# Performance work log

Measured on AMD Instinct MI355X. Metric: run time of the kernel, lower is better.

## Reference

```python
import jax, jax.numpy as jnp
import numpy as np

EMB = 256  # embedding_dim


def setup_inputs() -> dict:
    key = jax.random.key(0)
    ks = jax.random.split(key, 9)
    B, S, D = 4, 4096, EMB
    inputs = jax.random.normal(ks[0], (B, S, 3 * D), dtype=jnp.float32)
    def dense(kw, kb, d_in, d_out):
        w = jax.random.normal(kw, (d_in, d_out), dtype=jnp.float32) / np.sqrt(d_in)
        b = jnp.zeros((d_out,), dtype=jnp.float32)
        return w, b
    wq, bq = dense(ks[1], ks[2], D, D)
    wk, bk = dense(ks[3], ks[4], D, D)
    wv, bv = dense(ks[5], ks[6], D, D)
    wo, bo = dense(ks[7], ks[8], D, D)
    return {"inputs": inputs, "wq": wq, "bq": bq, "wk": wk, "bk": bk,
            "wv": wv, "bv": bv, "wo": wo, "bo": bo}


def reference(inputs, wq, bq, wk, bk, wv, bv, wo, bo):
    # split last axis into q,k,v parts: [B,S,D] each
    q_in, k_in, v_in = jnp.split(inputs, 3, axis=-1)
    q = q_in @ wq + bq
    k = k_in @ wk + bk
    v = v_in @ wv + bv
    dk = jnp.asarray(k.shape[-1], dtype=jnp.float32)
    # unfused SDPA exactly as source: matmul -> scale -> softmax -> matmul
    logits = jnp.einsum('bsd,btd->bst', q, k) / jnp.sqrt(dk)  # [B,S,S]
    attn = jax.nn.softmax(logits, axis=-1)
    x = jnp.einsum('bst,btd->bsd', attn, v)
    return x @ wo + bo
```

## Files before the change

### kernel.cpp

```cpp
#include <hip/hip_runtime.h>

typedef _Float16 f16;
typedef _Float16 f16x4 __attribute__((ext_vector_type(4)));
typedef _Float16 f16x8 __attribute__((ext_vector_type(8)));
typedef float f32x4  __attribute__((ext_vector_type(4)));

#define MFMAH(a, b, c) __builtin_amdgcn_mfma_f32_16x16x32_f16(a, b, c, 0, 0, 0)

constexpr int D = 256;
constexpr int S = 4096;
constexpr int BATCH = 4;
constexpr int NROWS = BATCH * S;
constexpr float SCALE = 0.0625f;
constexpr size_t NE = (size_t)NROWS * D;

__device__ __forceinline__ void gll16(const void* g, void* l) {
  __builtin_amdgcn_global_load_lds(
      (const __attribute__((address_space(1))) unsigned int*)g,
      (__attribute__((address_space(3))) unsigned int*)l, 16, 0, 0);
}

__global__ __launch_bounds__(256)
void prep_wt_kernel(const float* __restrict__ wq, const float* __restrict__ wk,
                    const float* __restrict__ wv, const float* __restrict__ wo,
                    f16* __restrict__ Wt)
{
  const int m = blockIdx.y;
  const float* w = (m == 0) ? wq : (m == 1) ? wk : (m == 2) ? wv : wo;
  int id = blockIdx.x * 256 + threadIdx.x;
  int n = id >> 8, k = id & 255;
  Wt[((size_t)m << 16) + n * 256 + k] = (f16)w[k * 256 + n];
}

__global__ __launch_bounds__(256)
void qkv_mfma_kernel(const float* __restrict__ in, const f16* __restrict__ Wt,
                     const float* __restrict__ bq, const float* __restrict__ bk,
                     const float* __restrict__ bv,
                     f16* __restrict__ Qh, f16* __restrict__ Kf, f16* __restrict__ Vf)
{
  __shared__ __align__(16) char smem[32768];
  const int m = blockIdx.y;
  const int tid = threadIdx.x, lane = tid & 63, w = tid >> 6;
  const int l15 = lane & 15, quad = lane >> 4;
  const int row0 = blockIdx.x * 64 + w * 16;
  const f16* Wm = Wt + ((size_t)m << 16);
  const float* bias = (m == 0) ? bq : (m == 1) ? bk : bv;

  f16x8 af[8];
  {
    const float* arow = in + (size_t)(row0 + l15) * 768 + m * 256 + quad * 8;
#pragma unroll
    for (int kc = 0; kc < 8; ++kc) {
      float4 a0 = *(const float4*)(arow + kc * 32);
      float4 a1 = *(const float4*)(arow + kc * 32 + 4);
      f16x8 a;
      a[0] = (f16)a0.x; a[1] = (f16)a0.y; a[2] = (f16)a0.z; a[3] = (f16)a0.w;
      a[4] = (f16)a1.x; a[5] = (f16)a1.y; a[6] = (f16)a1.z; a[7] = (f16)a1.w;
      af[kc] = a;
    }
  }

  auto stageB = [&](int buf, int kc) {
    char* base = smem + buf * 16384;
#pragma unroll
    for (int i = 0; i < 4; ++i) {
      int ct = 4 * w + i;
      gll16(Wm + (ct * 16 + l15) * 256 + kc * 32 + quad * 8,
            base + ct * 1024 + lane * 16);
    }
  };

  f32x4 acc[16];
#pragma unroll
  for (int ct = 0; ct < 16; ++ct) acc[ct] = (f32x4){0.f, 0.f, 0.f, 0.f};

  stageB(0, 0);
  for (int kc = 0; kc < 8; ++kc) {
    __syncthreads();
    if (kc < 7) stageB((kc + 1) & 1, kc + 1);
    const char* Bb = smem + (kc & 1) * 16384;
#pragma unroll
    for (int ct = 0; ct < 16; ++ct) {
      f16x8 b = *(const f16x8*)(Bb + ct * 1024 + lane * 16);
      acc[ct] = MFMAH(af[kc], b, acc[ct]);
    }
  }
  __syncthreads();

  const int b_ = row0 >> 12;

  if (m == 0) {
    f16* ws = (f16*)(smem + w * 8192);
#pragma unroll
    for (int ct = 0; ct < 16; ++ct) {
      float bct = bias[ct * 16 + l15];
#pragma unroll
      for (int r = 0; r < 4; ++r)
        ws[(quad * 4 + r) * 256 + ct * 16 + l15] = (f16)((acc[ct][r] + bct) * SCALE);
    }
    f16* dst = Qh + (size_t)row0 * 256;
#pragma unroll
    for (int i = 0; i < 8; ++i)
      *(uint4*)(dst + lane * 8 + i * 512) = *(const uint4*)(ws + lane * 8 + i * 512);
  } else if (m == 1) {
    f16* ws = (f16*)(smem + w * 8192);
#pragma unroll
    for (int ct = 0; ct < 16; ++ct) {
      float bct = bias[ct * 16 + l15];
      int base = (ct >> 1) * 512 + ((ct & 1) * 2 + (l15 >> 3)) * 128 + (l15 & 7);
#pragma unroll
      for (int r = 0; r < 4; ++r)
        ws[base + (quad * 4 + r) * 8] = (f16)(acc[ct][r] + bct);
    }
    const int g = (row0 & 4095) >> 4;
    f16* dst = Kf + ((size_t)(b_ * 256 + g)) * 8 * 512;
#pragma unroll
    for (int i = 0; i < 8; ++i)
      *(uint4*)(dst + lane * 8 + i * 512) = *(const uint4*)(ws + lane * 8 + i * 512);
  } else {
    const int t = w & 1;
    f16* ws = (f16*)(smem + (w >> 1) * 16384);
#pragma unroll
    for (int ct = 0; ct < 16; ++ct) {
      float bct = bias[ct * 16 + l15];
      int base = ct * 512 + quad * 128 + l15 * 8 + t * 4;
#pragma unroll
      for (int r = 0; r < 4; ++r)
        ws[base + r] = (f16)(acc[ct][r] + bct);
    }
    __syncthreads();
    const int gv0 = ((blockIdx.x * 64) & 4095) >> 5;
    f16* dst = Vf + ((size_t)(b_ * 128 + gv0)) * 16 * 512;
    const f16* src = (const f16*)smem;
#pragma unroll
    for (int i = 0; i < 8; ++i)
      *(uint4*)(dst + tid * 8 + i * 2048) = *(const uint4*)(src + tid * 8 + i * 2048);
  }
}

__global__ __launch_bounds__(256, 2)
void attn6_kernel(const f16* __restrict__ Qh, const char* __restrict__ Kf,
                  const char* __restrict__ Vf,
                  f16* __restrict__ Pp, float* __restrict__ Mp, float* __restrict__ Lp)
{
  __shared__ __align__(16) char KVs[2][32768];

  const int tid = threadIdx.x, lane = tid & 63, w = tid >> 6;
  const int l15 = lane & 15, quad = lane >> 4;

  const int bx    = blockIdx.x;
  const int combo = bx & 15;
  const int b     = combo & 3;
  const int kz    = combo >> 2;
  const int qb    = bx >> 4;
  const int qrow0 = qb * 128 + w * 32;
  const int grow  = b * 4096 + qrow0;

  f16x8 qf[2][8];
#pragma unroll
  for (int sub = 0; sub < 2; ++sub) {
    const size_t qoff = (size_t)(grow + sub * 16 + l15) * 256 + quad * 8;
#pragma unroll
    for (int kc = 0; kc < 8; ++kc)
      qf[sub][kc] = *(const f16x8*)(Qh + qoff + kc * 32);
  }

  const char* kg[4];
  const char* vg[4];
#pragma unroll
  for (int i = 0; i < 4; ++i) {
    int f = 4 * w + i;
    kg[i] = Kf + (((size_t)(b * 256 + kz * 64 + (f >> 3))) * 8 + (f & 7)) * 1024
               + lane * 16;
    vg[i] = Vf + (((size_t)(b * 128 + kz * 32)) * 16 + f) * 1024 + lane * 16;
  }
  auto stage = [&](int buf) {
    char* base = &KVs[buf][0];
#pragma unroll
    for (int i = 0; i < 4; ++i) { gll16(kg[i], base + (4 * w + i) * 1024); kg[i] += 16384; }
#pragma unroll
    for (int i = 0; i < 4; ++i) { gll16(vg[i], base + 16384 + (4 * w + i) * 1024); vg[i] += 16384; }
  };

  f32x4 o0[16], o1[16];
#pragma unroll
  for (int ct = 0; ct < 16; ++ct) {
    o0[ct] = (f32x4){0.f, 0.f, 0.f, 0.f};
    o1[ct] = (f32x4){0.f, 0.f, 0.f, 0.f};
  }
  float m0 = -3.0e38f, m1 = -3.0e38f, l0 = 0.f, l1 = 0.f;

  stage(0);

  for (int it = 0; it < 32; ++it) {
    __syncthreads();
    if (it < 31) stage((it + 1) & 1);
    const char* Bf = &KVs[it & 1][0];

    f32x4 sA0 = (f32x4){0.f,0.f,0.f,0.f}, sB0 = (f32x4){0.f,0.f,0.f,0.f};
    f32x4 sA1 = (f32x4){0.f,0.f,0.f,0.f}, sB1 = (f32x4){0.f,0.f,0.f,0.f};
#pragma unroll
    for (int kc = 0; kc < 8; ++kc) {
      f16x8 kA = *(const f16x8*)(Bf + kc * 1024 + lane * 16);
      f16x8 kB = *(const f16x8*)(Bf + 8192 + kc * 1024 + lane * 16);
      sA0 = MFMAH(kA, qf[0][kc], sA0);
      sA1 = MFMAH(kA, qf[1][kc], sA1);
      sB0 = MFMAH(kB, qf[0][kc], sB0);
      sB1 = MFMAH(kB, qf[1][kc], sB1);
    }

    float mn0, mn1, al0, al1;
    f16x8 ph0, ph1;
    {
      float t = fmaxf(fmaxf(fmaxf(sA0[0], sA0[1]), fmaxf(sA0[2], sA0[3])),
                      fmaxf(fmaxf(sB0[0], sB0[1]), fmaxf(sB0[2], sB0[3])));
      t = fmaxf(t, __shfl_xor(t, 16));
      t = fmaxf(t, __shfl_xor(t, 32));
      mn0 = fmaxf(m0, t);
      al0 = __expf(m0 - mn0);
      float ps = 0.f;
#pragma unroll
      for (int r = 0; r < 4; ++r) {
        float pa = __expf(sA0[r] - mn0);
        float pb = __expf(sB0[r] - mn0);
        ph0[r] = (f16)pa;  ph0[r + 4] = (f16)pb;
        ps += pa + pb;
      }
      ps += __shfl_xor(ps, 16);
      ps += __shfl_xor(ps, 32);
      l0 = l0 * al0 + ps;
    }
    {
      float t = fmaxf(fmaxf(fmaxf(sA1[0], sA1[1]), fmaxf(sA1[2], sA1[3])),
                      fmaxf(fmaxf(sB1[0], sB1[1]), fmaxf(sB1[2], sB1[3])));
      t = fmaxf(t, __shfl_xor(t, 16));
      t = fmaxf(t, __shfl_xor(t, 32));
      mn1 = fmaxf(m1, t);
      al1 = __expf(m1 - mn1);
      float ps = 0.f;
#pragma unroll
      for (int r = 0; r < 4; ++r) {
        float pa = __expf(sA1[r] - mn1);
        float pb = __expf(sB1[r] - mn1);
        ph1[r] = (f16)pa;  ph1[r + 4] = (f16)pb;
        ps += pa + pb;
      }
      ps += __shfl_xor(ps, 16);
      ps += __shfl_xor(ps, 32);
      l1 = l1 * al1 + ps;
    }

    if (__any(mn0 > m0)) {
      float a0 = __shfl(al0, (quad << 2) + 0);
      float a1 = __shfl(al0, (quad << 2) + 1);
      float a2 = __shfl(al0, (quad << 2) + 2);
      float a3 = __shfl(al0, (quad << 2) + 3);
#pragma unroll
      for (int ct = 0; ct < 16; ++ct) {
        o0[ct][0] *= a0; o0[ct][1] *= a1; o0[ct][2] *= a2; o0[ct][3] *= a3;
      }
    }
    if (__any(mn1 > m1)) {
      float a0 = __shfl(al1, (quad << 2) + 0);
      float a1 = __shfl(al1, (quad << 2) + 1);
      float a2 = __shfl(al1, (quad << 2) + 2);
      float a3 = __shfl(al1, (quad << 2) + 3);
#pragma unroll
      for (int ct = 0; ct < 16; ++ct) {
        o1[ct][0] *= a0; o1[ct][1] *= a1; o1[ct][2] *= a2; o1[ct][3] *= a3;
      }
    }
    m0 = mn0;  m1 = mn1;

#pragma unroll
    for (int ct = 0; ct < 16; ++ct) {
      f16x8 vf = *(const f16x8*)(Bf + 16384 + ct * 1024 + lane * 16);
      o0[ct] = MFMAH(ph0, vf, o0[ct]);
      o1[ct] = MFMAH(ph1, vf, o1[ct]);
    }
  }

  f16* Od = Pp + (size_t)kz * NE;
#pragma unroll
  for (int r = 0; r < 4; ++r) {
    const size_t ro0 = (size_t)(grow + quad * 4 + r) * 256 + l15;
    const size_t ro1 = (size_t)(grow + 16 + quad * 4 + r) * 256 + l15;
#pragma unroll
    for (int ct = 0; ct < 16; ++ct) {
      Od[ro0 + ct * 16] = (f16)o0[ct][r];
      Od[ro1 + ct * 16] = (f16)o1[ct][r];
    }
  }
  if (lane < 16) {
    Mp[kz * NROWS + grow + l15] = m0;
    Lp[kz * NROWS + grow + l15] = l0;
    Mp[kz * NROWS + grow + 16 + l15] = m1;
    Lp[kz * NROWS + grow + 16 + l15] = l1;
  }
}

__global__ __launch_bounds__(256)
void oproj_mfma_kernel(const f16* __restrict__ Pp, const float* __restrict__ Mp,
                       const float* __restrict__ Lp, const f16* __restrict__ Wto,
                       const float* __restrict__ bo, float* __restrict__ out)
{
  __shared__ f16 xs[32][264];
  __shared__ __align__(16) char Bs[2][16384];
  const int tid = threadIdx.x, lane = tid & 63, w = tid >> 6;
  const int l15 = lane & 15, quad = lane >> 4;
  const int rb = blockIdx.x * 32;

  auto stageB = [&](int buf, int kc) {
    char* base = &Bs[buf][0];
#pragma unroll
    for (int i = 0; i < 4; ++i) {
      int ct = 4 * w + i;
      gll16(Wto + (ct * 16 + l15) * 256 + kc * 32 + quad * 8,
            base + ct * 1024 + lane * 16);
    }
  };
  stageB(0, 0);

  const int c4 = (tid & 63) * 4;
  const int rsub = tid >> 6;
#pragma unroll
  for (int e = 0; e < 8; ++e) {
    int rl = e * 4 + rsub;
    int row = rb + rl;
    float m[4], l[4];
#pragma unroll
    for (int z = 0; z < 4; ++z) {
      m[z] = Mp[z * NROWS + row];
      l[z] = Lp[z * NROWS + row];
    }
    float mm = fmaxf(fmaxf(m[0], m[1]), fmaxf(m[2], m[3]));
    float wz[4], denom = 0.f;
#pragma unroll
    for (int z = 0; z < 4; ++z) { wz[z] = __expf(m[z] - mm); denom += wz[z] * l[z]; }
    float inv = 1.0f / denom;
    float s0 = 0.f, s1 = 0.f, s2 = 0.f, s3 = 0.f;
#pragma unroll
    for (int z = 0; z < 4; ++z) {
      f16x4 h = *(const f16x4*)(Pp + (size_t)z * NE + (size_t)row * 256 + c4);
      s0 += wz[z] * (float)h[0];
      s1 += wz[z] * (float)h[1];
      s2 += wz[z] * (float)h[2];
      s3 += wz[z] * (float)h[3];
    }
    f16x4 xv;
    xv[0] = (f16)(s0 * inv); xv[1] = (f16)(s1 * inv);
    xv[2] = (f16)(s2 * inv); xv[3] = (f16)(s3 * inv);
    *(f16x4*)&xs[rl][c4] = xv;
  }

  const int rw = (w & 1) * 16;
  const int cg = (w >> 1) * 8;
  f32x4 acc[8];
#pragma unroll
  for (int c = 0; c < 8; ++c) acc[c] = (f32x4){0.f, 0.f, 0.f, 0.f};

  for (int kc = 0; kc < 8; ++kc) {
    __syncthreads();
    if (kc < 7) stageB((kc + 1) & 1, kc + 1);
    const char* Bb = &Bs[kc & 1][0];
    f16x8 a = *(const f16x8*)&xs[rw + l15][kc * 32 + quad * 8];
#pragma unroll
    for (int c = 0; c < 8; ++c) {
      f16x8 b = *(const f16x8*)(Bb + (cg + c) * 1024 + lane * 16);
      acc[c] = MFMAH(a, b, acc[c]);
    }
  }

#pragma unroll
  for (int c = 0; c < 8; ++c) {
    int col = (cg + c) * 16 + l15;
    float bct = bo[col];
#pragma unroll
    for (int r = 0; r < 4; ++r)
      out[(size_t)(rb + rw + quad * 4 + r) * 256 + col] = acc[c][r] + bct;
  }
}

extern "C" void kernel_launch(void* const* d_in, const int* in_sizes, int n_in,
                              void* d_out, int out_size, void* d_ws, size_t ws_size,
                              hipStream_t stream)
{
  const float* inp = (const float*)d_in[0];
  const float* wq  = (const float*)d_in[1];
  const float* bq  = (const float*)d_in[2];
  const float* wk  = (const float*)d_in[3];
  const float* bk  = (const float*)d_in[4];
  const float* wv  = (const float*)d_in[5];
  const float* bv  = (const float*)d_in[6];
  const float* wo  = (const float*)d_in[7];
  const float* bo  = (const float*)d_in[8];
  float* out = (float*)d_out;

  f16* Qh = (f16*)d_ws;
  f16* Kf = Qh + NE;
  f16* Vf = Kf + NE;
  f16* Wt = Vf + NE;
  f16* Pp = Wt + 4 * 65536;
  float* Mp = (float*)(Pp + 4 * NE);
  float* Lp = Mp + 4 * NROWS;

  prep_wt_kernel<<<dim3(256, 4), 256, 0, stream>>>(wq, wk, wv, wo, Wt);

  qkv_mfma_kernel<<<dim3(256, 3), 256, 0, stream>>>(
      inp, Wt, bq, bk, bv, Qh, Kf, Vf);

  attn6_kernel<<<512, 256, 0, stream>>>(Qh, (const char*)Kf, (const char*)Vf,
                                        Pp, Mp, Lp);

  oproj_mfma_kernel<<<512, 256, 0, stream>>>(Pp, Mp, Lp, Wt + 3 * 65536, bo, out);
}
```

Baseline: 242.9 us.

## Use exp2 softmax, lazy max rescaling with threshold, and MFMA priority hints

Folds log2(e) into the score scale so the softmax uses the native exp2 instruction instead of __expf. It rescales the running max and output accumulators only when a new tile max exceeds the current max by more than a threshold, which skips most rescale passes. It also raises wave priority around the two MFMA loops to help matrix work interleave with the softmax of other waves. The lazy rescale lets unnormalised probabilities reach up to 2^6, which risks fp16 range and precision loss in the P values.

```diff
diff --git a/kernel.cpp b/kernel.cpp
--- a/kernel.cpp
+++ b/kernel.cpp
@@ -6,12 +6,14 @@
 typedef float f32x4  __attribute__((ext_vector_type(4)));
 
 #define MFMAH(a, b, c) __builtin_amdgcn_mfma_f32_16x16x32_f16(a, b, c, 0, 0, 0)
+#define EX2(x) __builtin_amdgcn_exp2f(x)
 
 constexpr int D = 256;
 constexpr int S = 4096;
 constexpr int BATCH = 4;
 constexpr int NROWS = BATCH * S;
-constexpr float SCALE = 0.0625f;
+constexpr float SCALE = 0.0625f * 1.44269504088896340736f;
+constexpr float DTHR = 6.0f;
 constexpr size_t NE = (size_t)NROWS * D;
 
 __device__ __forceinline__ void gll16(const void* g, void* l) {
@@ -199,6 +201,7 @@
 
     f32x4 sA0 = (f32x4){0.f,0.f,0.f,0.f}, sB0 = (f32x4){0.f,0.f,0.f,0.f};
     f32x4 sA1 = (f32x4){0.f,0.f,0.f,0.f}, sB1 = (f32x4){0.f,0.f,0.f,0.f};
+    __builtin_amdgcn_s_setprio(1);
 #pragma unroll
     for (int kc = 0; kc < 8; ++kc) {
       f16x8 kA = *(const f16x8*)(Bf + kc * 1024 + lane * 16);
@@ -208,76 +211,80 @@
       sB0 = MFMAH(kB, qf[0][kc], sB0);
       sB1 = MFMAH(kB, qf[1][kc], sB1);
     }
-
-    float mn0, mn1, al0, al1;
+    __builtin_amdgcn_s_setprio(0);
+
     f16x8 ph0, ph1;
     {
       float t = fmaxf(fmaxf(fmaxf(sA0[0], sA0[1]), fmaxf(sA0[2], sA0[3])),
                       fmaxf(fmaxf(sB0[0], sB0[1]), fmaxf(sB0[2], sB0[3])));
       t = fmaxf(t, __shfl_xor(t, 16));
       t = fmaxf(t, __shfl_xor(t, 32));
-      mn0 = fmaxf(m0, t);
-      al0 = __expf(m0 - mn0);
+      if (__any(t > m0 + DTHR)) {
+        float mn = fmaxf(m0, t);
+        float al = EX2(m0 - mn);
+        float a0 = __shfl(al, (quad << 2) + 0);
+        float a1 = __shfl(al, (quad << 2) + 1);
+        float a2 = __shfl(al, (quad << 2) + 2);
+        float a3 = __shfl(al, (quad << 2) + 3);
+#pragma unroll
+        for (int ct = 0; ct < 16; ++ct) {
+          o0[ct][0] *= a0; o0[ct][1] *= a1; o0[ct][2] *= a2; o0[ct][3] *= a3;
+        }
+        l0 *= al;
+        m0 = mn;
+      }
       float ps = 0.f;
 #pragma unroll
       for (int r = 0; r < 4; ++r) {
-        float pa = __expf(sA0[r] - mn0);
-        float pb = __expf(sB0[r] - mn0);
+        float pa = EX2(sA0[r] - m0);
+        float pb = EX2(sB0[r] - m0);
         ph0[r] = (f16)pa;  ph0[r + 4] = (f16)pb;
         ps += pa + pb;
       }
       ps += __shfl_xor(ps, 16);
       ps += __shfl_xor(ps, 32);
-      l0 = l0 * al0 + ps;
+      l0 += ps;
     }
     {
       float t = fmaxf(fmaxf(fmaxf(sA1[0], sA1[1]), fmaxf(sA1[2], sA1[3])),
                       fmaxf(fmaxf(sB1[0], sB1[1]), fmaxf(sB1[2], sB1[3])));
       t = fmaxf(t, __shfl_xor(t, 16));
       t = fmaxf(t, __shfl_xor(t, 32));
-      mn1 = fmaxf(m1, t);
-      al1 = __expf(m1 - mn1);
+      if (__any(t > m1 + DTHR)) {
+        float mn = fmaxf(m1, t);
+        float al = EX2(m1 - mn);
+        float a0 = __shfl(al, (quad << 2) + 0);
+        float a1 = __shfl(al, (quad << 2) + 1);
+        float a2 = __shfl(al, (quad << 2) + 2);
+        float a3 = __shfl(al, (quad << 2) + 3);
+#pragma unroll
+        for (int ct = 0; ct < 16; ++ct) {
+          o1[ct][0] *= a0; o1[ct][1] *= a1; o1[ct][2] *= a2; o1[ct][3] *= a3;
+        }
+        l1 *= al;
+        m1 = mn;
+      }
       float ps = 0.f;
 #pragma unroll
       for (int r = 0; r < 4; ++r) {
-        float pa = __expf(sA1[r] - mn1);
-        float pb = __expf(sB1[r] - mn1);
+        float pa = EX2(sA1[r] - m1);
+        float pb = EX2(sB1[r] - m1);
         ph1[r] = (f16)pa;  ph1[r + 4] = (f16)pb;
         ps += pa + pb;
       }
       ps += __shfl_xor(ps, 16);
       ps += __shfl_xor(ps, 32);
-      l1 = l1 * al1 + ps;
-    }
-
-    if (__any(mn0 > m0)) {
-      float a0 = __shfl(al0, (quad << 2) + 0);
-      float a1 = __shfl(al0, (quad << 2) + 1);
-      float a2 = __shfl(al0, (quad << 2) + 2);
-      float a3 = __shfl(al0, (quad << 2) + 3);
-#pragma unroll
-      for (int ct = 0; ct < 16; ++ct) {
-        o0[ct][0] *= a0; o0[ct][1] *= a1; o0[ct][2] *= a2; o0[ct][3] *= a3;
-      }
-    }
-    if (__any(mn1 > m1)) {
-      float a0 = __shfl(al1, (quad << 2) + 0);
-      float a1 = __shfl(al1, (quad << 2) + 1);
-      float a2 = __shfl(al1, (quad << 2) + 2);
-      float a3 = __shfl(al1, (quad << 2) + 3);
-#pragma unroll
-      for (int ct = 0; ct < 16; ++ct) {
-        o1[ct][0] *= a0; o1[ct][1] *= a1; o1[ct][2] *= a2; o1[ct][3] *= a3;
-      }
-    }
-    m0 = mn0;  m1 = mn1;
-
+      l1 += ps;
+    }
+
+    __builtin_amdgcn_s_setprio(1);
 #pragma unroll
     for (int ct = 0; ct < 16; ++ct) {
       f16x8 vf = *(const f16x8*)(Bf + 16384 + ct * 1024 + lane * 16);
       o0[ct] = MFMAH(ph0, vf, o0[ct]);
       o1[ct] = MFMAH(ph1, vf, o1[ct]);
     }
+    __builtin_amdgcn_s_setprio(0);
   }
 
   f16* Od = Pp + (size_t)kz * NE;
@@ -336,7 +343,7 @@
     float mm = fmaxf(fmaxf(m[0], m[1]), fmaxf(m[2], m[3]));
     float wz[4], denom = 0.f;
 #pragma unroll
-    for (int z = 0; z < 4; ++z) { wz[z] = __expf(m[z] - mm); denom += wz[z] * l[z]; }
+    for (int z = 0; z < 4; ++z) { wz[z] = EX2(m[z] - mm); denom += wz[z] * l[z]; }
     float inv = 1.0f / denom;
     float s0 = 0.f, s1 = 0.f, s2 = 0.f, s3 = 0.f;
 #pragma unroll
```

Result: faster. 214.3 us (-11.8%).
